# Kernel tuning notes

Hardware: AMD Instinct MI355X
Metric: run time of the kernel (lower is better)

Reference implementation:

```python
import jax, jax.numpy as jnp
from jax import lax
import numpy as np

B, N, NPOINT, NSAMPLE = 4, 8192, 1024, 32
RADIUS = 0.2
EPS = 1e-5
C_IN = 16
MLP_DIMS = [(3 + C_IN, 64), (64, 64), (64, 128)]


def setup_inputs() -> dict:
    key = jax.random.key(0)
    ks = jax.random.split(key, 16)
    inp = {
        "xyz": jax.random.uniform(ks[0], (B, N, 3), dtype=jnp.float32),
        "points": jax.random.normal(ks[1], (B, N, C_IN), dtype=jnp.float32),
    }
    for i, (cin, cout) in enumerate(MLP_DIMS, 1):
        inp[f"w{i}"] = jax.random.normal(ks[1 + i], (cout, cin), dtype=jnp.float32) / np.sqrt(cin)
        inp[f"b{i}"] = jnp.zeros((cout,), jnp.float32)
        inp[f"g{i}"] = jnp.ones((cout,), jnp.float32)
        inp[f"be{i}"] = jnp.zeros((cout,), jnp.float32)
    return inp


def fps(xyz, npoint):
    # Farthest point sampling; sequential by nature -> lax.scan over npoint steps.
    # Deterministic start at index 0 (torch version uses a random start).
    b, n, _ = xyz.shape
    def step(carry, _):
        dist, far = carry
        centroid = jnp.take_along_axis(xyz, far[:, None, None], axis=1)  # [B,1,3]
        d = jnp.sum((xyz - centroid) ** 2, -1)                            # [B,N]
        dist = jnp.minimum(dist, d)
        return (dist, jnp.argmax(dist, -1).astype(jnp.int32)), far
    init = (jnp.full((b, n), 1e10, xyz.dtype), jnp.zeros((b,), jnp.int32))
    _, idxs = lax.scan(step, init, None, length=npoint)
    return jnp.transpose(idxs)  # [B, npoint]


def gather2(pts, idx):  # pts [B,N,C], idx [B,S] -> [B,S,C]
    return jnp.take_along_axis(pts, idx[..., None], axis=1)


def gather3(pts, idx):  # pts [B,N,C], idx [B,S,K] -> [B,S,K,C]
    b, s, k = idx.shape
    out = jnp.take_along_axis(pts, idx.reshape(b, s * k)[..., None], axis=1)
    return out.reshape(b, s, k, pts.shape[-1])


def ball_query(radius, nsample, xyz, new_xyz):
    n = xyz.shape[1]
    # [B,S,N] pairwise squared distances (the memory-bound hot spot)
    sqr = jnp.sum((new_xyz[:, :, None, :] - xyz[:, None, :, :]) ** 2, -1)
    gidx = jnp.where(sqr > radius * radius, n, jnp.arange(n, dtype=jnp.int32))
    gidx = jnp.sort(gidx, axis=-1)[:, :, :nsample]
    first = gidx[:, :, :1]
    return jnp.where(gidx == n, first, gidx)


def mlp_layer(x, w, b, g, be):
    # 1x1 Conv2d + BatchNorm2d (train mode: batch stats over B,S,K) + ReLU
    y = jnp.einsum('bskc,oc->bsko', x, w) + b
    mu = jnp.mean(y, axis=(0, 1, 2))
    var = jnp.var(y, axis=(0, 1, 2))
    y = (y - mu) * (g * lax.rsqrt(var + EPS)) + be
    return jax.nn.relu(y)


def reference(xyz, points, w1, b1, g1, be1, w2, b2, g2, be2, w3, b3, g3, be3):
    fps_idx = fps(xyz, NPOINT)                       # [B,S]
    new_xyz = gather2(xyz, fps_idx)                  # [B,S,3]
    idx = ball_query(RADIUS, NSAMPLE, xyz, new_xyz)  # [B,S,K]
    grouped_xyz_norm = gather3(xyz, idx) - new_xyz[:, :, None, :]  # [B,S,K,3]
    grouped_points = gather3(points, idx)            # [B,S,K,C]
    feat = jnp.concatenate([grouped_xyz_norm, grouped_points], -1)  # [B,S,K,3+C]
    feat = mlp_layer(feat, w1, b1, g1, be1)
    feat = mlp_layer(feat, w2, b2, g2, be2)
    feat = mlp_layer(feat, w3, b3, g3, be3)
    new_points = jnp.max(feat, axis=2)               # max-pool over neighbors -> [B,S,128]
    return new_xyz, new_points
```

## Files before the change

### kernel.cpp

```cpp
#include <hip/hip_runtime.h>

#define NB 4
#define NP 8192
#define NS 1024
#define NK 32
#define CNT_ALL 131072.0f

typedef float v2f __attribute__((ext_vector_type(2)));

template <int CTRL>
__device__ __forceinline__ unsigned dpp_max_u32(unsigned m)
{
    unsigned o = (unsigned)__builtin_amdgcn_update_dpp((int)m, (int)m, CTRL, 0xF, 0xF, false);
    return (o > m) ? o : m;
}

template <int CTRL>
__device__ __forceinline__ unsigned long long dpp_max_u64(unsigned long long k)
{
    unsigned lo = (unsigned)k, hi = (unsigned)(k >> 32);
    unsigned olo = (unsigned)__builtin_amdgcn_update_dpp((int)lo, (int)lo, CTRL, 0xF, 0xF, false);
    unsigned ohi = (unsigned)__builtin_amdgcn_update_dpp((int)hi, (int)hi, CTRL, 0xF, 0xF, false);
    unsigned long long o = ((unsigned long long)ohi << 32) | (unsigned long long)olo;
    return (o > k) ? o : k;
}

__global__ __launch_bounds__(512, 2) void fps_kernel(const float* __restrict__ xyz,
                                                     float* __restrict__ newxyz,
                                                     float* __restrict__ st)
{
#pragma clang fp contract(off)
    if (blockIdx.x >= NB) {
        for (int i = threadIdx.x; i < 4096; i += 512) st[i] = 0.f;
        return;
    }
    const int b = blockIdx.x;
    const int tid = threadIdx.x;
    const int lane = tid & 63;
    const int w = tid >> 6;
    const float* xb = xyz + (size_t)b * NP * 3;

    __shared__ float s_px[NP], s_py[NP], s_pz[NP];
    __shared__ unsigned long long s_kv[2][8];

#pragma unroll
    for (int k = 0; k < 16; ++k) {
        const int i = k * 512 + tid;
        s_px[i] = xb[3 * i + 0];
        s_py[i] = xb[3 * i + 1];
        s_pz[i] = xb[3 * i + 2];
    }
    __syncthreads();

    v2f px[8], py[8], pz[8], dist[8];
    const int base = tid << 4;
#pragma unroll
    for (int m = 0; m < 8; ++m) {
        const int p0 = base + 2 * m;
        px[m] = v2f{s_px[p0], s_px[p0 + 1]};
        py[m] = v2f{s_py[p0], s_py[p0 + 1]};
        pz[m] = v2f{s_pz[p0], s_pz[p0 + 1]};
        dist[m] = v2f{1e10f, 1e10f};
    }
    float cx = s_px[0], cy = s_py[0], cz = s_pz[0];
    float* ob = newxyz + (size_t)b * NS * 3;

    for (int it = 0; it < NS; ++it) {
        if (tid == 0) { ob[it * 3 + 0] = cx; ob[it * 3 + 1] = cy; ob[it * 3 + 2] = cz; }
        const v2f cxx = v2f{cx, cx}, cyy = v2f{cy, cy}, czz = v2f{cz, cz};
        float bd0 = -1.0f, bd1 = -1.0f;
        int bj0 = 0, bj1 = 0;
#pragma unroll
        for (int m = 0; m < 8; ++m) {
            v2f dx = px[m] - cxx, dy = py[m] - cyy, dz = pz[m] - czz;
            v2f d = (dx * dx + dy * dy) + dz * dz;
            float d0 = fminf(dist[m].x, d.x);
            float d1 = fminf(dist[m].y, d.y);
            dist[m].x = d0;
            dist[m].y = d1;
            bool t0 = d0 > bd0;
            bd0 = t0 ? d0 : bd0;
            bj0 = t0 ? 2 * m : bj0;
            bool t1 = d1 > bd1;
            bd1 = t1 ? d1 : bd1;
            bj1 = t1 ? 2 * m + 1 : bj1;
        }
        const bool tm = (bd1 > bd0) || ((bd1 == bd0) && (bj1 < bj0));
        const float bd = tm ? bd1 : bd0;
        const int ibest = base + (tm ? bj1 : bj0);
        const unsigned ub = __float_as_uint(bd);
        unsigned m0 = dpp_max_u32<0xB1>(ub);
        m0 = dpp_max_u32<0x4E>(m0);
        m0 = dpp_max_u32<0x141>(m0);
        m0 = dpp_max_u32<0x140>(m0);
        m0 = dpp_max_u32<0x142>(m0);
        m0 = dpp_max_u32<0x143>(m0);
        const unsigned maxbits = (unsigned)__builtin_amdgcn_readlane((int)m0, 63);
        const unsigned long long bm = __ballot(ub == maxbits);
        const int srclane = __ffsll(bm) - 1;
        const int wbi = __builtin_amdgcn_readlane(ibest, srclane);
        if (lane == 0)
            s_kv[it & 1][w] = ((unsigned long long)maxbits << 32) | (unsigned)(NP - 1 - wbi);
        __syncthreads();
        unsigned long long kv = s_kv[it & 1][lane & 7];
        kv = dpp_max_u64<0xB1>(kv);
        kv = dpp_max_u64<0x4E>(kv);
        kv = dpp_max_u64<0x141>(kv);
        const int fi = NP - 1 - (int)(unsigned)(kv & 0xFFFFFFFFull);
        cx = s_px[fi]; cy = s_py[fi]; cz = s_pz[fi];
    }
}

__device__ __forceinline__ void bn_coef(const float* __restrict__ sums,
                                        const float* __restrict__ sqs,
                                        const float* __restrict__ g,
                                        const float* __restrict__ be,
                                        int C, int c, float& sc, float& sh)
{
    float s = 0.f, q = 0.f;
#pragma unroll
    for (int k = 0; k < 8; ++k) { s += sums[k * C + c]; q += sqs[k * C + c]; }
    const float mean = s / CNT_ALL;
    const float var = q / CNT_ALL - mean * mean;
    sc = g[c] / sqrtf(var + 1e-5f);
    sh = be[c] - mean * sc;
}

__global__ __launch_bounds__(256) void phaseA_kernel(
    const float* __restrict__ xyz, const float* __restrict__ pts,
    const float* __restrict__ newxyz,
    const float* __restrict__ w1, const float* __restrict__ b1,
    float* __restrict__ y1, float* __restrict__ st)
{
    __shared__ int   s_ball[8][NK];
    __shared__ float s_feat[256][20];
    __shared__ float s_ps[256], s_pq[256];
    float* sums1 = st;
    float* sqs1 = st + 512;

    const int tid = threadIdx.x;
    const int bk = blockIdx.x;
    const int lane = tid & 63;
    const int wv_id = tid >> 6;

    const int b = (8 * bk) >> 10;
    const float* xb = xyz + (size_t)b * NP * 3;
    const float rr = (float)(0.2 * 0.2);
    for (int r = 0; r < 2; ++r) {
        const int lg = 2 * wv_id + r;
        const int sg = 8 * bk + lg;
        const float cx = newxyz[sg * 3 + 0];
        const float cy = newxyz[sg * 3 + 1];
        const float cz = newxyz[sg * 3 + 2];
        int cnt = 0;
        for (int base = 0; base < NP && cnt < NK; base += 64) {
            const int p = base + lane;
            float dx = xb[p * 3 + 0] - cx;
            float dy = xb[p * 3 + 1] - cy;
            float dz = xb[p * 3 + 2] - cz;
            float d = __fadd_rn(__fadd_rn(__fmul_rn(dx, dx), __fmul_rn(dy, dy)),
                                __fmul_rn(dz, dz));
            bool in = (d <= rr);
            unsigned long long mask = __ballot(in);
            int before = __popcll(mask & ((1ull << lane) - 1ull));
            int pos = cnt + before;
            if (in && pos < NK) s_ball[lg][pos] = p;
            cnt += (int)__popcll(mask);
        }
        cnt = min(cnt, NK);
        const int v0 = s_ball[lg][0];
        if (lane < NK && lane >= cnt) s_ball[lg][lane] = v0;
    }
    __syncthreads();
    {
        const int lg = tid >> 5, k = tid & 31;
        const int id = s_ball[lg][k];
        const int sg = 8 * bk + lg;
        const float* pp = xyz + ((size_t)b * NP + id) * 3;
        const float* cp = newxyz + (size_t)sg * 3;
        float* f = s_feat[tid];
        f[0] = pp[0] - cp[0];
        f[1] = pp[1] - cp[1];
        f[2] = pp[2] - cp[2];
        const float4* q4 = (const float4*)(pts + ((size_t)b * NP + id) * 16);
#pragma unroll
        for (int i = 0; i < 4; ++i) {
            float4 v = q4[i];
            f[3 + 4 * i + 0] = v.x; f[3 + 4 * i + 1] = v.y;
            f[3 + 4 * i + 2] = v.z; f[3 + 4 * i + 3] = v.w;
        }
        f[19] = 0.f;
    }
    __syncthreads();
    const int c = tid & 63, rg = tid >> 6;
    float wv[20];
#pragma unroll
    for (int j = 0; j < 19; ++j) wv[j] = w1[c * 19 + j];
    wv[19] = 0.f;
    const float bs = b1[c];
    float s = 0.f, q = 0.f;
    for (int r = 0; r < 64; ++r) {
        const int row = rg * 64 + r;
        const float4* f4 = (const float4*)s_feat[row];
        float acc = bs;
#pragma unroll
        for (int j4 = 0; j4 < 5; ++j4) {
            float4 v = f4[j4];
            acc += wv[4*j4+0]*v.x + wv[4*j4+1]*v.y + wv[4*j4+2]*v.z + wv[4*j4+3]*v.w;
        }
        y1[((size_t)256 * bk + row) * 64 + c] = acc;
        s += acc; q += acc * acc;
    }
    s_ps[tid] = s; s_pq[tid] = q;
    __syncthreads();
    if (rg == 0) {
        float ts = s_ps[c] + s_ps[64 + c] + s_ps[128 + c] + s_ps[192 + c];
        float tq = s_pq[c] + s_pq[64 + c] + s_pq[128 + c] + s_pq[192 + c];
        atomicAdd(&sums1[(bk & 7) * 64 + c], ts);
        atomicAdd(&sqs1[(bk & 7) * 64 + c], tq);
    }
}

__global__ __launch_bounds__(256) void phaseB_kernel(
    const float* __restrict__ y1,
    const float* __restrict__ g1, const float* __restrict__ be1,
    const float* __restrict__ w2, const float* __restrict__ b2,
    float* __restrict__ y2, float* __restrict__ st)
{
    __shared__ float x_lds[128 * 64];
    __shared__ float s_sc[64], s_sh[64];
    __shared__ float s_ps[256], s_pq[256];
    const float* sums1 = st;
    const float* sqs1 = st + 512;
    float* sums2 = st + 1024;
    float* sqs2 = st + 1536;

    const int tid = threadIdx.x;
    const int bk = blockIdx.x;
    if (tid < 64) {
        float sc, sh;
        bn_coef(sums1, sqs1, g1, be1, 64, tid, sc, sh);
        s_sc[tid] = sc; s_sh[tid] = sh;
    }
    __syncthreads();
    const int c = tid & 63, rg = tid >> 6;
    float wv[64];
#pragma unroll
    for (int j = 0; j < 64; ++j) wv[j] = w2[c * 64 + j];
    const float bs = b2[c];
    float s = 0.f, q = 0.f;
    for (int half = 0; half < 2; ++half) {
        const size_t row0 = (size_t)256 * bk + 128 * half;
        const float4* y1g = (const float4*)(y1 + row0 * 64);
        float4* xl4 = (float4*)x_lds;
#pragma unroll
        for (int i = 0; i < 8; ++i) {
            const int slot = i * 256 + tid;
            float4 v = y1g[slot];
            const int c4 = (slot & 15) * 4;
            float4 o;
            o.x = fmaxf(v.x * s_sc[c4+0] + s_sh[c4+0], 0.f);
            o.y = fmaxf(v.y * s_sc[c4+1] + s_sh[c4+1], 0.f);
            o.z = fmaxf(v.z * s_sc[c4+2] + s_sh[c4+2], 0.f);
            o.w = fmaxf(v.w * s_sc[c4+3] + s_sh[c4+3], 0.f);
            xl4[slot] = o;
        }
        __syncthreads();
        for (int r = 0; r < 32; ++r) {
            const int row = rg * 32 + r;
            const float4* x4 = (const float4*)(x_lds + row * 64);
            float acc = bs;
#pragma unroll
            for (int j4 = 0; j4 < 16; ++j4) {
                float4 v = x4[j4];
                acc += wv[4*j4+0]*v.x + wv[4*j4+1]*v.y + wv[4*j4+2]*v.z + wv[4*j4+3]*v.w;
            }
            y2[(row0 + row) * 64 + c] = acc;
            s += acc; q += acc * acc;
        }
        __syncthreads();
    }
    s_ps[tid] = s; s_pq[tid] = q;
    __syncthreads();
    if (rg == 0) {
        float ts = s_ps[c] + s_ps[64 + c] + s_ps[128 + c] + s_ps[192 + c];
        float tq = s_pq[c] + s_pq[64 + c] + s_pq[128 + c] + s_pq[192 + c];
        atomicAdd(&sums2[(bk & 7) * 64 + c], ts);
        atomicAdd(&sqs2[(bk & 7) * 64 + c], tq);
    }
}

__global__ __launch_bounds__(256) void phaseC_kernel(
    const float* __restrict__ y2,
    const float* __restrict__ g2, const float* __restrict__ be2,
    const float* __restrict__ w3, const float* __restrict__ b3,
    float* __restrict__ st)
{
    __shared__ float s_x[NK * 64];
    __shared__ float s_sc[64], s_sh[64];
    __shared__ float s_p3s[256], s_p3q[256];
    const float* sums2 = st + 1024;
    const float* sqs2 = st + 1536;
    float* sums3 = st + 2048;
    float* sqs3 = st + 3072;

    const int tid = threadIdx.x;
    const int bk = blockIdx.x;
    if (tid < 64) {
        float sc, sh;
        bn_coef(sums2, sqs2, g2, be2, 64, tid, sc, sh);
        s_sc[tid] = sc; s_sh[tid] = sh;
    }
    __syncthreads();
    const int c = tid & 127, rg = tid >> 7;
    float wv[64];
#pragma unroll
    for (int j = 0; j < 64; ++j) wv[j] = w3[c * 64 + j];
    const float bs = b3[c];
    float s = 0.f, q = 0.f;
    for (int gi = 0; gi < 8; ++gi) {
        const size_t grow0 = (size_t)256 * bk + 32 * gi;
        const float4* y2g = (const float4*)(y2 + grow0 * 64);
        float4* sx4 = (float4*)s_x;
#pragma unroll
        for (int i = 0; i < 2; ++i) {
            const int slot = i * 256 + tid;
            float4 v = y2g[slot];
            const int c4 = (slot & 15) * 4;
            float4 o;
            o.x = fmaxf(v.x * s_sc[c4+0] + s_sh[c4+0], 0.f);
            o.y = fmaxf(v.y * s_sc[c4+1] + s_sh[c4+1], 0.f);
            o.z = fmaxf(v.z * s_sc[c4+2] + s_sh[c4+2], 0.f);
            o.w = fmaxf(v.w * s_sc[c4+3] + s_sh[c4+3], 0.f);
            sx4[slot] = o;
        }
        __syncthreads();
        for (int r = 0; r < 16; ++r) {
            const int row = rg * 16 + r;
            const float4* x4 = (const float4*)(s_x + row * 64);
            float acc = bs;
#pragma unroll
            for (int j4 = 0; j4 < 16; ++j4) {
                float4 v = x4[j4];
                acc += wv[4*j4+0]*v.x + wv[4*j4+1]*v.y + wv[4*j4+2]*v.z + wv[4*j4+3]*v.w;
            }
            s += acc; q += acc * acc;
        }
        __syncthreads();
    }
    s_p3s[rg * 128 + c] = s; s_p3q[rg * 128 + c] = q;
    __syncthreads();
    if (rg == 0) {
        atomicAdd(&sums3[(bk & 7) * 128 + c], s_p3s[c] + s_p3s[128 + c]);
        atomicAdd(&sqs3[(bk & 7) * 128 + c], s_p3q[c] + s_p3q[128 + c]);
    }
}

__global__ __launch_bounds__(256) void phaseD_kernel(
    const float* __restrict__ y2,
    const float* __restrict__ g2, const float* __restrict__ be2,
    const float* __restrict__ g3, const float* __restrict__ be3,
    const float* __restrict__ w3, const float* __restrict__ b3,
    const float* __restrict__ st, float* __restrict__ out_np)
{
    __shared__ float s_x[NK * 64];
    __shared__ float s_sc[64], s_sh[64];
    __shared__ float s_fm[256];
    const float* sums2 = st + 1024;
    const float* sqs2 = st + 1536;
    const float* sums3 = st + 2048;
    const float* sqs3 = st + 3072;

    const int tid = threadIdx.x;
    const int bk = blockIdx.x;
    if (tid < 64) {
        float sc, sh;
        bn_coef(sums2, sqs2, g2, be2, 64, tid, sc, sh);
        s_sc[tid] = sc; s_sh[tid] = sh;
    }
    const int c = tid & 127, rg = tid >> 7;
    float sc3, sh3;
    bn_coef(sums3, sqs3, g3, be3, 128, c, sc3, sh3);
    __syncthreads();
    float wv[64];
#pragma unroll
    for (int j = 0; j < 64; ++j) wv[j] = w3[c * 64 + j];
    const float bs = b3[c];
    for (int gi = 0; gi < 8; ++gi) {
        const size_t grow0 = (size_t)256 * bk + 32 * gi;
        const float4* y2g = (const float4*)(y2 + grow0 * 64);
        float4* sx4 = (float4*)s_x;
#pragma unroll
        for (int i = 0; i < 2; ++i) {
            const int slot = i * 256 + tid;
            float4 v = y2g[slot];
            const int c4 = (slot & 15) * 4;
            float4 o;
            o.x = fmaxf(v.x * s_sc[c4+0] + s_sh[c4+0], 0.f);
            o.y = fmaxf(v.y * s_sc[c4+1] + s_sh[c4+1], 0.f);
            o.z = fmaxf(v.z * s_sc[c4+2] + s_sh[c4+2], 0.f);
            o.w = fmaxf(v.w * s_sc[c4+3] + s_sh[c4+3], 0.f);
            sx4[slot] = o;
        }
        __syncthreads();
        float m = 0.f;
        for (int r = 0; r < 16; ++r) {
            const int row = rg * 16 + r;
            const float4* x4 = (const float4*)(s_x + row * 64);
            float acc = bs;
#pragma unroll
            for (int j4 = 0; j4 < 16; ++j4) {
                float4 v = x4[j4];
                acc += wv[4*j4+0]*v.x + wv[4*j4+1]*v.y + wv[4*j4+2]*v.z + wv[4*j4+3]*v.w;
            }
            float rv = fmaxf(acc * sc3 + sh3, 0.f);
            m = fmaxf(m, rv);
        }
        s_fm[rg * 128 + c] = m;
        __syncthreads();
        if (rg == 0)
            out_np[(size_t)(8 * bk + gi) * 128 + c] = fmaxf(s_fm[c], s_fm[128 + c]);
        __syncthreads();
    }
}

extern "C" void kernel_launch(void* const* d_in, const int* in_sizes, int n_in,
                              void* d_out, int out_size, void* d_ws, size_t ws_size,
                              hipStream_t stream)
{
    (void)in_sizes; (void)n_in; (void)out_size;
    const float* xyz = (const float*)d_in[0];
    const float* pts = (const float*)d_in[1];
    const float* w1 = (const float*)d_in[2];
    const float* b1 = (const float*)d_in[3];
    const float* g1 = (const float*)d_in[4];
    const float* be1 = (const float*)d_in[5];
    const float* w2 = (const float*)d_in[6];
    const float* b2 = (const float*)d_in[7];
    const float* g2 = (const float*)d_in[8];
    const float* be2 = (const float*)d_in[9];
    const float* w3 = (const float*)d_in[10];
    const float* b3 = (const float*)d_in[11];
    const float* g3 = (const float*)d_in[12];
    const float* be3 = (const float*)d_in[13];

    float* out = (float*)d_out;
    float* newxyz = out;
    float* newpts = out + NB * NS * 3;

    float* y1 = (float*)d_ws;
    float* y2 = y1 + 8388608;
    float* st = y2 + 8388608;
    const size_t needed = (2ull * 8388608ull + 4096ull) * 4ull;
    if (ws_size < needed) return;

    fps_kernel<<<NB + 1, 512, 0, stream>>>(xyz, newxyz, st);
    phaseA_kernel<<<512, 256, 0, stream>>>(xyz, pts, newxyz, w1, b1, y1, st);
    phaseB_kernel<<<512, 256, 0, stream>>>(y1, g1, be1, w2, b2, y2, st);
    phaseC_kernel<<<512, 256, 0, stream>>>(y2, g2, be2, w3, b3, st);
    phaseD_kernel<<<512, 256, 0, stream>>>(y2, g2, be2, g3, be3, w3, b3, st, newpts);
}
```

Before: 1.123 ms.

## Fuse MLP phase kernels into one persistent kernel with grid barriers

Merges the four per-layer kernels (ball query + layer1, layer2, layer3 stats, layer3 + maxpool) into a single kernel launch. The phases are separated by atomic-counter grid barriers, and batch-norm statistics are read with agent-scope atomic loads. This is meant to remove kernel launch gaps and per-launch ramp-up and tail costs. It relies on all 512 blocks being co-resident; otherwise it deadlocks. Spin-wait barriers also add some overhead.

```diff
diff --git a/kernel.cpp b/kernel.cpp
--- a/kernel.cpp
+++ b/kernel.cpp
@@ -5,6 +5,7 @@
 #define NS 1024
 #define NK 32
 #define CNT_ALL 131072.0f
+#define NBLK 512
 
 typedef float v2f __attribute__((ext_vector_type(2)));
 
@@ -31,7 +32,7 @@
 {
 #pragma clang fp contract(off)
     if (blockIdx.x >= NB) {
-        for (int i = threadIdx.x; i < 4096; i += 512) st[i] = 0.f;
+        for (int i = threadIdx.x; i < 4104; i += 512) st[i] = 0.f;
         return;
     }
     const int b = blockIdx.x;
@@ -111,316 +112,318 @@
     }
 }
 
-__device__ __forceinline__ void bn_coef(const float* __restrict__ sums,
-                                        const float* __restrict__ sqs,
-                                        const float* __restrict__ g,
-                                        const float* __restrict__ be,
-                                        int C, int c, float& sc, float& sh)
+__device__ __forceinline__ float aload(const float* p)
+{
+    return __hip_atomic_load((float*)p, __ATOMIC_RELAXED, __HIP_MEMORY_SCOPE_AGENT);
+}
+
+__device__ __forceinline__ void bn_coef_a(const float* __restrict__ sums,
+                                          const float* __restrict__ sqs,
+                                          const float* __restrict__ g,
+                                          const float* __restrict__ be,
+                                          int C, int c, float& sc, float& sh)
 {
     float s = 0.f, q = 0.f;
 #pragma unroll
-    for (int k = 0; k < 8; ++k) { s += sums[k * C + c]; q += sqs[k * C + c]; }
+    for (int k = 0; k < 8; ++k) { s += aload(&sums[k * C + c]); q += aload(&sqs[k * C + c]); }
     const float mean = s / CNT_ALL;
     const float var = q / CNT_ALL - mean * mean;
     sc = g[c] / sqrtf(var + 1e-5f);
     sh = be[c] - mean * sc;
 }
 
-__global__ __launch_bounds__(256) void phaseA_kernel(
+__device__ __forceinline__ void gridbar(unsigned* ctr)
+{
+    __syncthreads();
+    if (threadIdx.x == 0) {
+        __threadfence();
+        __hip_atomic_fetch_add(ctr, 1u, __ATOMIC_RELEASE, __HIP_MEMORY_SCOPE_AGENT);
+        while (__hip_atomic_load(ctr, __ATOMIC_ACQUIRE, __HIP_MEMORY_SCOPE_AGENT) < NBLK)
+            __builtin_amdgcn_s_sleep(8);
+        __threadfence();
+    }
+    __syncthreads();
+}
+
+__global__ __launch_bounds__(256, 2) void fused_kernel(
     const float* __restrict__ xyz, const float* __restrict__ pts,
     const float* __restrict__ newxyz,
     const float* __restrict__ w1, const float* __restrict__ b1,
-    float* __restrict__ y1, float* __restrict__ st)
-{
-    __shared__ int   s_ball[8][NK];
-    __shared__ float s_feat[256][20];
-    __shared__ float s_ps[256], s_pq[256];
-    float* sums1 = st;
-    float* sqs1 = st + 512;
-
+    const float* __restrict__ g1, const float* __restrict__ be1,
+    const float* __restrict__ w2, const float* __restrict__ b2,
+    const float* __restrict__ g2, const float* __restrict__ be2,
+    const float* __restrict__ w3, const float* __restrict__ b3,
+    const float* __restrict__ g3, const float* __restrict__ be3,
+    float* __restrict__ y1, float* __restrict__ y2,
+    float* __restrict__ st, float* __restrict__ out_np)
+{
+    __shared__ __align__(16) char smem[36864];
     const int tid = threadIdx.x;
     const int bk = blockIdx.x;
     const int lane = tid & 63;
     const int wv_id = tid >> 6;
 
-    const int b = (8 * bk) >> 10;
-    const float* xb = xyz + (size_t)b * NP * 3;
-    const float rr = (float)(0.2 * 0.2);
-    for (int r = 0; r < 2; ++r) {
-        const int lg = 2 * wv_id + r;
-        const int sg = 8 * bk + lg;
-        const float cx = newxyz[sg * 3 + 0];
-        const float cy = newxyz[sg * 3 + 1];
-        const float cz = newxyz[sg * 3 + 2];
-        int cnt = 0;
-        for (int base = 0; base < NP && cnt < NK; base += 64) {
-            const int p = base + lane;
-            float dx = xb[p * 3 + 0] - cx;
-            float dy = xb[p * 3 + 1] - cy;
-            float dz = xb[p * 3 + 2] - cz;
-            float d = __fadd_rn(__fadd_rn(__fmul_rn(dx, dx), __fmul_rn(dy, dy)),
-                                __fmul_rn(dz, dz));
-            bool in = (d <= rr);
-            unsigned long long mask = __ballot(in);
-            int before = __popcll(mask & ((1ull << lane) - 1ull));
-            int pos = cnt + before;
-            if (in && pos < NK) s_ball[lg][pos] = p;
-            cnt += (int)__popcll(mask);
-        }
-        cnt = min(cnt, NK);
-        const int v0 = s_ball[lg][0];
-        if (lane < NK && lane >= cnt) s_ball[lg][lane] = v0;
-    }
-    __syncthreads();
+    float* sums1 = st;            float* sqs1 = st + 512;
+    float* sums2 = st + 1024;     float* sqs2 = st + 1536;
+    float* sums3 = st + 2048;     float* sqs3 = st + 3072;
+    unsigned* ctr = (unsigned*)(st + 4096);
+
     {
-        const int lg = tid >> 5, k = tid & 31;
-        const int id = s_ball[lg][k];
-        const int sg = 8 * bk + lg;
-        const float* pp = xyz + ((size_t)b * NP + id) * 3;
-        const float* cp = newxyz + (size_t)sg * 3;
-        float* f = s_feat[tid];
-        f[0] = pp[0] - cp[0];
-        f[1] = pp[1] - cp[1];
-        f[2] = pp[2] - cp[2];
-        const float4* q4 = (const float4*)(pts + ((size_t)b * NP + id) * 16);
-#pragma unroll
-        for (int i = 0; i < 4; ++i) {
-            float4 v = q4[i];
-            f[3 + 4 * i + 0] = v.x; f[3 + 4 * i + 1] = v.y;
-            f[3 + 4 * i + 2] = v.z; f[3 + 4 * i + 3] = v.w;
-        }
-        f[19] = 0.f;
-    }
-    __syncthreads();
-    const int c = tid & 63, rg = tid >> 6;
-    float wv[20];
-#pragma unroll
-    for (int j = 0; j < 19; ++j) wv[j] = w1[c * 19 + j];
-    wv[19] = 0.f;
-    const float bs = b1[c];
-    float s = 0.f, q = 0.f;
-    for (int r = 0; r < 64; ++r) {
-        const int row = rg * 64 + r;
-        const float4* f4 = (const float4*)s_feat[row];
-        float acc = bs;
-#pragma unroll
-        for (int j4 = 0; j4 < 5; ++j4) {
-            float4 v = f4[j4];
-            acc += wv[4*j4+0]*v.x + wv[4*j4+1]*v.y + wv[4*j4+2]*v.z + wv[4*j4+3]*v.w;
-        }
-        y1[((size_t)256 * bk + row) * 64 + c] = acc;
-        s += acc; q += acc * acc;
-    }
-    s_ps[tid] = s; s_pq[tid] = q;
-    __syncthreads();
-    if (rg == 0) {
-        float ts = s_ps[c] + s_ps[64 + c] + s_ps[128 + c] + s_ps[192 + c];
-        float tq = s_pq[c] + s_pq[64 + c] + s_pq[128 + c] + s_pq[192 + c];
-        atomicAdd(&sums1[(bk & 7) * 64 + c], ts);
-        atomicAdd(&sqs1[(bk & 7) * 64 + c], tq);
-    }
-}
-
-__global__ __launch_bounds__(256) void phaseB_kernel(
-    const float* __restrict__ y1,
-    const float* __restrict__ g1, const float* __restrict__ be1,
-    const float* __restrict__ w2, const float* __restrict__ b2,
-    float* __restrict__ y2, float* __restrict__ st)
-{
-    __shared__ float x_lds[128 * 64];
-    __shared__ float s_sc[64], s_sh[64];
-    __shared__ float s_ps[256], s_pq[256];
-    const float* sums1 = st;
-    const float* sqs1 = st + 512;
-    float* sums2 = st + 1024;
-    float* sqs2 = st + 1536;
-
-    const int tid = threadIdx.x;
-    const int bk = blockIdx.x;
-    if (tid < 64) {
-        float sc, sh;
-        bn_coef(sums1, sqs1, g1, be1, 64, tid, sc, sh);
-        s_sc[tid] = sc; s_sh[tid] = sh;
-    }
-    __syncthreads();
-    const int c = tid & 63, rg = tid >> 6;
-    float wv[64];
-#pragma unroll
-    for (int j = 0; j < 64; ++j) wv[j] = w2[c * 64 + j];
-    const float bs = b2[c];
-    float s = 0.f, q = 0.f;
-    for (int half = 0; half < 2; ++half) {
-        const size_t row0 = (size_t)256 * bk + 128 * half;
-        const float4* y1g = (const float4*)(y1 + row0 * 64);
-        float4* xl4 = (float4*)x_lds;
-#pragma unroll
-        for (int i = 0; i < 8; ++i) {
-            const int slot = i * 256 + tid;
-            float4 v = y1g[slot];
-            const int c4 = (slot & 15) * 4;
-            float4 o;
-            o.x = fmaxf(v.x * s_sc[c4+0] + s_sh[c4+0], 0.f);
-            o.y = fmaxf(v.y * s_sc[c4+1] + s_sh[c4+1], 0.f);
-            o.z = fmaxf(v.z * s_sc[c4+2] + s_sh[c4+2], 0.f);
-            o.w = fmaxf(v.w * s_sc[c4+3] + s_sh[c4+3], 0.f);
-            xl4[slot] = o;
-        }
-        __syncthreads();
-        for (int r = 0; r < 32; ++r) {
-            const int row = rg * 32 + r;
-            const float4* x4 = (const float4*)(x_lds + row * 64);
+        int*   s_ball = (int*)smem;
+        float* s_feat = (float*)(smem + 1024);
+        float* s_ps   = (float*)(smem + 1024 + 20480);
+        float* s_pq   = s_ps + 256;
+
+        const int b = (8 * bk) >> 10;
+        const float* xb = xyz + (size_t)b * NP * 3;
+        const float rr = (float)(0.2 * 0.2);
+        for (int r = 0; r < 2; ++r) {
+            const int lg = 2 * wv_id + r;
+            const int sg = 8 * bk + lg;
+            const float cx = newxyz[sg * 3 + 0];
+            const float cy = newxyz[sg * 3 + 1];
+            const float cz = newxyz[sg * 3 + 2];
+            int cnt = 0;
+            for (int base = 0; base < NP && cnt < NK; base += 64) {
+                const int p = base + lane;
+                float dx = xb[p * 3 + 0] - cx;
+                float dy = xb[p * 3 + 1] - cy;
+                float dz = xb[p * 3 + 2] - cz;
+                float d = __fadd_rn(__fadd_rn(__fmul_rn(dx, dx), __fmul_rn(dy, dy)),
+                                    __fmul_rn(dz, dz));
+                bool in = (d <= rr);
+                unsigned long long mask = __ballot(in);
+                int before = __popcll(mask & ((1ull << lane) - 1ull));
+                int pos = cnt + before;
+                if (in && pos < NK) s_ball[lg * NK + pos] = p;
+                cnt += (int)__popcll(mask);
+            }
+            cnt = min(cnt, NK);
+            const int v0 = s_ball[lg * NK];
+            if (lane < NK && lane >= cnt) s_ball[lg * NK + lane] = v0;
+        }
+        __syncthreads();
+        {
+            const int lg = tid >> 5, k = tid & 31;
+            const int id = s_ball[lg * NK + k];
+            const int sg = 8 * bk + lg;
+            const float* pp = xyz + ((size_t)b * NP + id) * 3;
+            const float* cp = newxyz + (size_t)sg * 3;
+            float* f = s_feat + tid * 20;
+            f[0] = pp[0] - cp[0];
+            f[1] = pp[1] - cp[1];
+            f[2] = pp[2] - cp[2];
+            const float4* q4 = (const float4*)(pts + ((size_t)b * NP + id) * 16);
+#pragma unroll
+            for (int i = 0; i < 4; ++i) {
+                float4 v = q4[i];
+                f[3 + 4 * i + 0] = v.x; f[3 + 4 * i + 1] = v.y;
+                f[3 + 4 * i + 2] = v.z; f[3 + 4 * i + 3] = v.w;
+            }
+            f[19] = 0.f;
+        }
+        __syncthreads();
+        const int c = tid & 63, rg = tid >> 6;
+        float wv[20];
+#pragma unroll
+        for (int j = 0; j < 19; ++j) wv[j] = w1[c * 19 + j];
+        wv[19] = 0.f;
+        const float bs = b1[c];
+        float s = 0.f, q = 0.f;
+        for (int r = 0; r < 64; ++r) {
+            const int row = rg * 64 + r;
+            const float4* f4 = (const float4*)(s_feat + row * 20);
             float acc = bs;
 #pragma unroll
-            for (int j4 = 0; j4 < 16; ++j4) {
-                float4 v = x4[j4];
+            for (int j4 = 0; j4 < 5; ++j4) {
+                float4 v = f4[j4];
                 acc += wv[4*j4+0]*v.x + wv[4*j4+1]*v.y + wv[4*j4+2]*v.z + wv[4*j4+3]*v.w;
             }
-            y2[(row0 + row) * 64 + c] = acc;
+            y1[((size_t)256 * bk + row) * 64 + c] = acc;
             s += acc; q += acc * acc;
         }
-        __syncthreads();
-    }
-    s_ps[tid] = s; s_pq[tid] = q;
-    __syncthreads();
-    if (rg == 0) {
-        float ts = s_ps[c] + s_ps[64 + c] + s_ps[128 + c] + s_ps[192 + c];
-        float tq = s_pq[c] + s_pq[64 + c] + s_pq[128 + c] + s_pq[192 + c];
-        atomicAdd(&sums2[(bk & 7) * 64 + c], ts);
-        atomicAdd(&sqs2[(bk & 7) * 64 + c], tq);
-    }
-}
-
-__global__ __launch_bounds__(256) void phaseC_kernel(
-    const float* __restrict__ y2,
-    const float* __restrict__ g2, const float* __restrict__ be2,
-    const float* __restrict__ w3, const float* __restrict__ b3,
-    float* __restrict__ st)
-{
-    __shared__ float s_x[NK * 64];
-    __shared__ float s_sc[64], s_sh[64];
-    __shared__ float s_p3s[256], s_p3q[256];
-    const float* sums2 = st + 1024;
-    const float* sqs2 = st + 1536;
-    float* sums3 = st + 2048;
-    float* sqs3 = st + 3072;
-
-    const int tid = threadIdx.x;
-    const int bk = blockIdx.x;
-    if (tid < 64) {
-        float sc, sh;
-        bn_coef(sums2, sqs2, g2, be2, 64, tid, sc, sh);
-        s_sc[tid] = sc; s_sh[tid] = sh;
-    }
-    __syncthreads();
-    const int c = tid & 127, rg = tid >> 7;
-    float wv[64];
-#pragma unroll
-    for (int j = 0; j < 64; ++j) wv[j] = w3[c * 64 + j];
-    const float bs = b3[c];
-    float s = 0.f, q = 0.f;
-    for (int gi = 0; gi < 8; ++gi) {
-        const size_t grow0 = (size_t)256 * bk + 32 * gi;
-        const float4* y2g = (const float4*)(y2 + grow0 * 64);
-        float4* sx4 = (float4*)s_x;
-#pragma unroll
-        for (int i = 0; i < 2; ++i) {
-            const int slot = i * 256 + tid;
-            float4 v = y2g[slot];
-            const int c4 = (slot & 15) * 4;
-            float4 o;
-            o.x = fmaxf(v.x * s_sc[c4+0] + s_sh[c4+0], 0.f);
-            o.y = fmaxf(v.y * s_sc[c4+1] + s_sh[c4+1], 0.f);
-            o.z = fmaxf(v.z * s_sc[c4+2] + s_sh[c4+2], 0.f);
-            o.w = fmaxf(v.w * s_sc[c4+3] + s_sh[c4+3], 0.f);
-            sx4[slot] = o;
-        }
-        __syncthreads();
-        for (int r = 0; r < 16; ++r) {
-            const int row = rg * 16 + r;
-            const float4* x4 = (const float4*)(s_x + row * 64);
-            float acc = bs;
-#pragma unroll
-            for (int j4 = 0; j4 < 16; ++j4) {
-                float4 v = x4[j4];
-                acc += wv[4*j4+0]*v.x + wv[4*j4+1]*v.y + wv[4*j4+2]*v.z + wv[4*j4+3]*v.w;
-            }
-            s += acc; q += acc * acc;
-        }
-        __syncthreads();
-    }
-    s_p3s[rg * 128 + c] = s; s_p3q[rg * 128 + c] = q;
-    __syncthreads();
-    if (rg == 0) {
-        atomicAdd(&sums3[(bk & 7) * 128 + c], s_p3s[c] + s_p3s[128 + c]);
-        atomicAdd(&sqs3[(bk & 7) * 128 + c], s_p3q[c] + s_p3q[128 + c]);
-    }
-}
-
-__global__ __launch_bounds__(256) void phaseD_kernel(
-    const float* __restrict__ y2,
-    const float* __restrict__ g2, const float* __restrict__ be2,
-    const float* __restrict__ g3, const float* __restrict__ be3,
-    const float* __restrict__ w3, const float* __restrict__ b3,
-    const float* __restrict__ st, float* __restrict__ out_np)
-{
-    __shared__ float s_x[NK * 64];
-    __shared__ float s_sc[64], s_sh[64];
-    __shared__ float s_fm[256];
-    const float* sums2 = st + 1024;
-    const float* sqs2 = st + 1536;
-    const float* sums3 = st + 2048;
-    const float* sqs3 = st + 3072;
-
-    const int tid = threadIdx.x;
-    const int bk = blockIdx.x;
-    if (tid < 64) {
-        float sc, sh;
-        bn_coef(sums2, sqs2, g2, be2, 64, tid, sc, sh);
-        s_sc[tid] = sc; s_sh[tid] = sh;
-    }
-    const int c = tid & 127, rg = tid >> 7;
-    float sc3, sh3;
-    bn_coef(sums3, sqs3, g3, be3, 128, c, sc3, sh3);
-    __syncthreads();
-    float wv[64];
-#pragma unroll
-    for (int j = 0; j < 64; ++j) wv[j] = w3[c * 64 + j];
-    const float bs = b3[c];
-    for (int gi = 0; gi < 8; ++gi) {
-        const size_t grow0 = (size_t)256 * bk + 32 * gi;
-        const float4* y2g = (const float4*)(y2 + grow0 * 64);
-        float4* sx4 = (float4*)s_x;
-#pragma unroll
-        for (int i = 0; i < 2; ++i) {
-            const int slot = i * 256 + tid;
-            float4 v = y2g[slot];
-            const int c4 = (slot & 15) * 4;
-            float4 o;
-            o.x = fmaxf(v.x * s_sc[c4+0] + s_sh[c4+0], 0.f);
-            o.y = fmaxf(v.y * s_sc[c4+1] + s_sh[c4+1], 0.f);
-            o.z = fmaxf(v.z * s_sc[c4+2] + s_sh[c4+2], 0.f);
-            o.w = fmaxf(v.w * s_sc[c4+3] + s_sh[c4+3], 0.f);
-            sx4[slot] = o;
-        }
-        __syncthreads();
-        float m = 0.f;
-        for (int r = 0; r < 16; ++r) {
-            const int row = rg * 16 + r;
-            const float4* x4 = (const float4*)(s_x + row * 64);
-            float acc = bs;
-#pragma unroll
-            for (int j4 = 0; j4 < 16; ++j4) {
-                float4 v = x4[j4];
-                acc += wv[4*j4+0]*v.x + wv[4*j4+1]*v.y + wv[4*j4+2]*v.z + wv[4*j4+3]*v.w;
-            }
-            float rv = fmaxf(acc * sc3 + sh3, 0.f);
-            m = fmaxf(m, rv);
-        }
-        s_fm[rg * 128 + c] = m;
-        __syncthreads();
-        if (rg == 0)
-            out_np[(size_t)(8 * bk + gi) * 128 + c] = fmaxf(s_fm[c], s_fm[128 + c]);
-        __syncthreads();
+        s_ps[tid] = s; s_pq[tid] = q;
+        __syncthreads();
+        if (rg == 0) {
+            float ts = s_ps[c] + s_ps[64 + c] + s_ps[128 + c] + s_ps[192 + c];
+            float tq = s_pq[c] + s_pq[64 + c] + s_pq[128 + c] + s_pq[192 + c];
+            atomicAdd(&sums1[(bk & 7) * 64 + c], ts);
+            atomicAdd(&sqs1[(bk & 7) * 64 + c], tq);
+        }
+    }
+    gridbar(&ctr[0]);
+
+    {
+        float* x_lds = (float*)smem;
+        float* s_sc  = (float*)(smem + 32768);
+        float* s_sh  = s_sc + 64;
+        float* s_ps  = (float*)(smem + 32768 + 512);
+        float* s_pq  = s_ps + 256;
+        if (tid < 64) {
+            float sc, sh;
+            bn_coef_a(sums1, sqs1, g1, be1, 64, tid, sc, sh);
+            s_sc[tid] = sc; s_sh[tid] = sh;
+        }
+        __syncthreads();
+        const int c = tid & 63, rg = tid >> 6;
+        float wv[64];
+#pragma unroll
+        for (int j = 0; j < 64; ++j) wv[j] = w2[c * 64 + j];
+        const float bs = b2[c];
+        float s = 0.f, q = 0.f;
+        for (int half = 0; half < 2; ++half) {
+            const size_t row0 = (size_t)256 * bk + 128 * half;
+            const float4* y1g = (const float4*)(y1 + row0 * 64);
+            float4* xl4 = (float4*)x_lds;
+#pragma unroll
+            for (int i = 0; i < 8; ++i) {
+                const int slot = i * 256 + tid;
+                float4 v = y1g[slot];
+                const int c4 = (slot & 15) * 4;
+                float4 o;
+                o.x = fmaxf(v.x * s_sc[c4+0] + s_sh[c4+0], 0.f);
+                o.y = fmaxf(v.y * s_sc[c4+1] + s_sh[c4+1], 0.f);
+                o.z = fmaxf(v.z * s_sc[c4+2] + s_sh[c4+2], 0.f);
+                o.w = fmaxf(v.w * s_sc[c4+3] + s_sh[c4+3], 0.f);
+                xl4[slot] = o;
+            }
+            __syncthreads();
+            for (int r = 0; r < 32; ++r) {
+                const int row = rg * 32 + r;
+                const float4* x4 = (const float4*)(x_lds + row * 64);
+                float acc = bs;
+#pragma unroll
+                for (int j4 = 0; j4 < 16; ++j4) {
+                    float4 v = x4[j4];
+                    acc += wv[4*j4+0]*v.x + wv[4*j4+1]*v.y + wv[4*j4+2]*v.z + wv[4*j4+3]*v.w;
+                }
+                y2[(row0 + row) * 64 + c] = acc;
+                s += acc; q += acc * acc;
+            }
+            __syncthreads();
+        }
+        s_ps[tid] = s; s_pq[tid] = q;
+        __syncthreads();
+        if (rg == 0) {
+            float ts = s_ps[c] + s_ps[64 + c] + s_ps[128 + c] + s_ps[192 + c];
+            float tq = s_pq[c] + s_pq[64 + c] + s_pq[128 + c] + s_pq[192 + c];
+            atomicAdd(&sums2[(bk & 7) * 64 + c], ts);
+            atomicAdd(&sqs2[(bk & 7) * 64 + c], tq);
+        }
+    }
+    gridbar(&ctr[1]);
+
+    {
+        float* s_x  = (float*)smem;
+        float* s_sc = (float*)(smem + 32768);
+        float* s_sh = s_sc + 64;
+        float* s_p3s = (float*)(smem + 32768 + 512);
+        float* s_p3q = s_p3s + 256;
+        if (tid < 64) {
+            float sc, sh;
+            bn_coef_a(sums2, sqs2, g2, be2, 64, tid, sc, sh);
+            s_sc[tid] = sc; s_sh[tid] = sh;
+        }
+        __syncthreads();
+        const int c = tid & 127, rg = tid >> 7;
+        float wv[64];
+#pragma unroll
+        for (int j = 0; j < 64; ++j) wv[j] = w3[c * 64 + j];
+        const float bs = b3[c];
+        float s = 0.f, q = 0.f;
+        for (int gi = 0; gi < 8; ++gi) {
+            const size_t grow0 = (size_t)256 * bk + 32 * gi;
+            const float4* y2g = (const float4*)(y2 + grow0 * 64);
+            float4* sx4 = (float4*)s_x;
+#pragma unroll
+            for (int i = 0; i < 2; ++i) {
+                const int slot = i * 256 + tid;
+                float4 v = y2g[slot];
+                const int c4 = (slot & 15) * 4;
+                float4 o;
+                o.x = fmaxf(v.x * s_sc[c4+0] + s_sh[c4+0], 0.f);
+                o.y = fmaxf(v.y * s_sc[c4+1] + s_sh[c4+1], 0.f);
+                o.z = fmaxf(v.z * s_sc[c4+2] + s_sh[c4+2], 0.f);
+                o.w = fmaxf(v.w * s_sc[c4+3] + s_sh[c4+3], 0.f);
+                sx4[slot] = o;
+            }
+            __syncthreads();
+            for (int r = 0; r < 16; ++r) {
+                const int row = rg * 16 + r;
+                const float4* x4 = (const float4*)(s_x + row * 64);
+                float acc = bs;
+#pragma unroll
+                for (int j4 = 0; j4 < 16; ++j4) {
+                    float4 v = x4[j4];
+                    acc += wv[4*j4+0]*v.x + wv[4*j4+1]*v.y + wv[4*j4+2]*v.z + wv[4*j4+3]*v.w;
+                }
+                s += acc; q += acc * acc;
+            }
+            __syncthreads();
+        }
+        s_p3s[rg * 128 + c] = s; s_p3q[rg * 128 + c] = q;
+        __syncthreads();
+        if (rg == 0) {
+            atomicAdd(&sums3[(bk & 7) * 128 + c], s_p3s[c] + s_p3s[128 + c]);
+            atomicAdd(&sqs3[(bk & 7) * 128 + c], s_p3q[c] + s_p3q[128 + c]);
+        }
+    }
+    gridbar(&ctr[2]);
+
+    {
+        float* s_x  = (float*)smem;
+        float* s_sc = (float*)(smem + 32768);
+        float* s_sh = s_sc + 64;
+        float* s_fm = (float*)(smem + 32768 + 512);
+        if (tid < 64) {
+            float sc, sh;
+            bn_coef_a(sums2, sqs2, g2, be2, 64, tid, sc, sh);
+            s_sc[tid] = sc; s_sh[tid] = sh;
+        }
+        const int c = tid & 127, rg = tid >> 7;
+        float sc3, sh3;
+        bn_coef_a(sums3, sqs3, g3, be3, 128, c, sc3, sh3);
+        __syncthreads();
+        float wv[64];
+#pragma unroll
+        for (int j = 0; j < 64; ++j) wv[j] = w3[c * 64 + j];
+        const float bs = b3[c];
+        for (int gi = 0; gi < 8; ++gi) {
+            const size_t grow0 = (size_t)256 * bk + 32 * gi;
+            const float4* y2g = (const float4*)(y2 + grow0 * 64);
+            float4* sx4 = (float4*)s_x;
+#pragma unroll
+            for (int i = 0; i < 2; ++i) {
+                const int slot = i * 256 + tid;
+                float4 v = y2g[slot];
+                const int c4 = (slot & 15) * 4;
+                float4 o;
+                o.x = fmaxf(v.x * s_sc[c4+0] + s_sh[c4+0], 0.f);
+                o.y = fmaxf(v.y * s_sc[c4+1] + s_sh[c4+1], 0.f);
+                o.z = fmaxf(v.z * s_sc[c4+2] + s_sh[c4+2], 0.f);
+                o.w = fmaxf(v.w * s_sc[c4+3] + s_sh[c4+3], 0.f);
+                sx4[slot] = o;
+            }
+            __syncthreads();
+            float m = 0.f;
+            for (int r = 0; r < 16; ++r) {
+                const int row = rg * 16 + r;
+                const float4* x4 = (const float4*)(s_x + row * 64);
+                float acc = bs;
+#pragma unroll
+                for (int j4 = 0; j4 < 16; ++j4) {
+                    float4 v = x4[j4];
+                    acc += wv[4*j4+0]*v.x + wv[4*j4+1]*v.y + wv[4*j4+2]*v.z + wv[4*j4+3]*v.w;
+                }
+                float rv = fmaxf(acc * sc3 + sh3, 0.f);
+                m = fmaxf(m, rv);
+            }
+            s_fm[rg * 128 + c] = m;
+            __syncthreads();
+            if (rg == 0)
+                out_np[(size_t)(8 * bk + gi) * 128 + c] = fmaxf(s_fm[c], s_fm[128 + c]);
+            __syncthreads();
+        }
     }
 }
 
@@ -451,12 +454,13 @@
     float* y1 = (float*)d_ws;
     float* y2 = y1 + 8388608;
     float* st = y2 + 8388608;
-    const size_t needed = (2ull * 8388608ull + 4096ull) * 4ull;
+    const size_t needed = (2ull * 8388608ull + 4352ull) * 4ull;
     if (ws_size < needed) return;
 
     fps_kernel<<<NB + 1, 512, 0, stream>>>(xyz, newxyz, st);
-    phaseA_kernel<<<512, 256, 0, stream>>>(xyz, pts, newxyz, w1, b1, y1, st);
-    phaseB_kernel<<<512, 256, 0, stream>>>(y1, g1, be1, w2, b2, y2, st);
-    phaseC_kernel<<<512, 256, 0, stream>>>(y2, g2, be2, w3, b3, st);
-    phaseD_kernel<<<512, 256, 0, stream>>>(y2, g2, be2, g3, be3, w3, b3, st, newpts);
-}
+    fused_kernel<<<NBLK, 256, 0, stream>>>(xyz, pts, newxyz,
+                                           w1, b1, g1, be1,
+                                           w2, b2, g2, be2,
+                                           w3, b3, g3, be3,
+                                           y1, y2, st, newpts);
+}
```

Result: slower. 1.394 ms (+24.2%).
